# Kernel tuning notes

Hardware: AMD Instinct MI355X
Metric: run time of the kernel (lower is better)

## Reference

```python
import jax, jax.numpy as jnp
import numpy as np

N_SPK = 2048
M_UTT = 16
D_EMB = 512
EPS = 1e-8  # torch cosine_similarity eps


def setup_inputs() -> dict:
    key = jax.random.key(0)
    k1, = jax.random.split(key, 1)
    speaker_vectors = jax.random.normal(k1, (N_SPK * M_UTT, D_EMB), dtype=jnp.float32)
    return {
        "speaker_vectors": speaker_vectors,
        "w": jnp.float32(10.0),
        "b": jnp.float32(-5.0),
        "speakers": N_SPK,
    }


def _normalize(x):
    # torch.cosine_similarity clamps each norm at eps
    n = jnp.maximum(jnp.linalg.norm(x, axis=-1, keepdims=True), EPS)
    return x / n


def reference(speaker_vectors, w, b, speakers):
    N = speakers
    NM, D = speaker_vectors.shape
    M = NM // N
    v3 = speaker_vectors.reshape(N, M, D)
    ssum = v3.sum(axis=1)                         # [N, D] per-speaker sums
    C = ssum / M                                  # full centroids [N, D]
    C_min = (ssum[:, None, :] - v3) / (M - 1)     # leave-one-out centroids [N, M, D]

    vn = _normalize(speaker_vectors)              # [NM, D]
    # diagonal similarities: cos(C_min[j], v[j]) per utterance j
    S_diag = jnp.sum(_normalize(C_min.reshape(NM, D)) * vn, axis=-1)  # [NM]
    # full similarity matrix via one normalized matmul: [N, NM]
    S_full = _normalize(C) @ vn.T
    # replace each speaker's own block row entries with leave-one-out sims
    col_spk = jnp.arange(NM) // M                 # speaker id of each column
    same = col_spk[None, :] == jnp.arange(N)[:, None]  # [N, NM]
    S = jnp.where(same, S_diag[None, :], S_full)

    # L_j = -(w*S_diag_j + b) + log sum_n exp(w*S[n,j] + b)
    L = -(w * S_diag + b) + jax.nn.logsumexp(w * S + b, axis=0)
    return L.sum()
```

## Files before the change

### kernel.cpp

```cpp
#include <hip/hip_runtime.h>
#include <stdint.h>

#define N_SPK 2048
#define M_UTT 16
#define D_EMB 512
#define NM (N_SPK * M_UTT)
#define FP8_SCALE 16.0f

typedef __attribute__((ext_vector_type(4))) float f32x4;
typedef __attribute__((ext_vector_type(4))) int   i32x4;
typedef __attribute__((ext_vector_type(8))) int   i32x8;

__device__ __forceinline__ void async_copy16(const void* g, void* l) {
    __builtin_amdgcn_global_load_lds(
        (const __attribute__((address_space(1))) unsigned int*)g,
        (__attribute__((address_space(3))) unsigned int*)l,
        16, 0, 0);
}

__device__ __forceinline__ i32x8 ld_frag(const unsigned char* base, int s0) {
    i32x4 lo = *(const i32x4*)(base + s0 * 16);
    i32x4 hi = *(const i32x4*)(base + (s0 ^ 1) * 16);
    return __builtin_shufflevector(lo, hi, 0, 1, 2, 3, 4, 5, 6, 7);
}

__global__ __launch_bounds__(256) void prep_kernel(
    const float* __restrict__ V, const float* __restrict__ wp,
    const float* __restrict__ bp, unsigned char* __restrict__ Cn8,
    unsigned char* __restrict__ vn8, float* __restrict__ dterm,
    float* __restrict__ colsum, float* __restrict__ out)
{
    const int spk = blockIdx.x, t = threadIdx.x;
    const int wave = t >> 6, lane = t & 63;
    const float2* vb = (const float2*)(V + (size_t)spk * (M_UTT * D_EMB));

    __shared__ __align__(16) float red[32][264];
    __shared__ float red2[32];
    __shared__ float invs[M_UTT];
    __shared__ float wred[4];

    if (spk < 128) colsum[spk * 256 + t] = 0.f;
    if (spk == 0 && t == 0) out[0] = 0.f;

    float2 p[M_UTT];
#pragma unroll
    for (int m = 0; m < M_UTT; ++m) p[m] = vb[m * 256 + t];

    float2 ss = make_float2(0.f, 0.f);
#pragma unroll
    for (int m = 0; m < M_UTT; ++m) { ss.x += p[m].x; ss.y += p[m].y; }

    float cnp = ss.x * ss.x + ss.y * ss.y;
#pragma unroll
    for (int off = 32; off > 0; off >>= 1) cnp += __shfl_xor(cnp, off);
    if (lane == 0) wred[wave] = cnp;

#pragma unroll
    for (int m = 0; m < M_UTT; ++m) {
        red[m][t]         = ss.x * p[m].x + ss.y * p[m].y;
        red[m + M_UTT][t] = p[m].x * p[m].x + p[m].y * p[m].y;
    }
    __syncthreads();
    const float cn2 = wred[0] + wred[1] + wred[2] + wred[3];

    {
        const int r = t >> 3, s = t & 7;
        const float4* rp = (const float4*)red;
        float4 a = make_float4(0.f, 0.f, 0.f, 0.f);
#pragma unroll
        for (int k = 0; k < 8; ++k) {
            float4 q = rp[r * 66 + s + 8 * k];
            a.x += q.x; a.y += q.y; a.z += q.z; a.w += q.w;
        }
        float v1 = (a.x + a.y) + (a.z + a.w);
        v1 += __shfl_xor(v1, 1);
        v1 += __shfl_xor(v1, 2);
        v1 += __shfl_xor(v1, 4);
        if (s == 0) red2[r] = v1;
    }
    __syncthreads();

    if (t < M_UTT) {
        const float sv = red2[t], vv = red2[t + M_UTT];
        const float cc = cn2 - 2.f * sv + vv;
        const float cv = sv - vv;
        const float dc = fmaxf(sqrtf(fmaxf(cc, 0.f)) * (1.f / (M_UTT - 1)), 1e-8f) * (M_UTT - 1);
        const float dv = fmaxf(sqrtf(vv), 1e-8f);
        dterm[spk * M_UTT + t] = (*wp) * (cv / (dc * dv)) + (*bp);
        invs[t] = FP8_SCALE / dv;
    }
    __syncthreads();

    const float cs = FP8_SCALE / (M_UTT * fmaxf(sqrtf(cn2) * (1.f / M_UTT), 1e-8f));
    {
        int pk = __builtin_amdgcn_cvt_pk_fp8_f32(ss.x * cs, ss.y * cs, 0, false);
        ((unsigned short*)(Cn8 + (size_t)spk * D_EMB))[t] = (unsigned short)pk;
    }
#pragma unroll
    for (int m = 0; m < M_UTT; ++m) {
        const float iv = invs[m];
        int pk = __builtin_amdgcn_cvt_pk_fp8_f32(p[m].x * iv, p[m].y * iv, 0, false);
        ((unsigned short*)(vn8 + ((size_t)(spk * M_UTT + m)) * D_EMB))[t] = (unsigned short)pk;
    }
}

__global__ __launch_bounds__(256) void gemm_kernel(
    const unsigned char* __restrict__ Cn8, const unsigned char* __restrict__ vn8,
    const float* __restrict__ wp, const float* __restrict__ bp,
    float* __restrict__ colsum)
{
    __shared__ __align__(16) unsigned char As[2][128 * 128];
    __shared__ __align__(16) unsigned char Bs[2][128 * 128];
    __shared__ float csum[128];

    const int tid = threadIdx.x;
    const int w = tid >> 6, l = tid & 63;
    const int by = blockIdx.x;
    const int bx = blockIdx.y;
    const float wgt = (*wp) * (1.f / (FP8_SCALE * FP8_SCALE));
    const float bsc = *bp;

    if (tid < 128) csum[tid] = 0.f;

    const int srow = w * 32 + (l >> 3);
    const int sg   = (l & 7) ^ ((l >> 3) & 7);
    const unsigned char* Ab = Cn8 + (size_t)(by * 128 + srow) * D_EMB + sg * 16;
    const unsigned char* Bb = vn8 + (size_t)(bx * 128 + srow) * D_EMB + sg * 16;
    const int woff = (w * 32) * 128;

    const int wm = w & 1, wn = w >> 1;
    const int l16 = l & 15, q = l >> 4;
    const int s0 = (2 * q) ^ (l & 7);
    const int rdoff = (wm * 64 + l16) * 128;
    const int rdoffB = (wn * 64 + l16) * 128;

    f32x4 acc[4][4];
    const f32x4 z = {0.f, 0.f, 0.f, 0.f};
#pragma unroll
    for (int i = 0; i < 4; ++i)
#pragma unroll
        for (int j = 0; j < 4; ++j) acc[i][j] = z;

#pragma unroll
    for (int i = 0; i < 4; ++i) {
        async_copy16(Ab + (size_t)(i * 8) * D_EMB, &As[0][woff + i * 1024]);
        async_copy16(Bb + (size_t)(i * 8) * D_EMB, &Bs[0][woff + i * 1024]);
    }
    __syncthreads();

#pragma unroll
    for (int it = 0; it < 4; ++it) {
        const int cur = it & 1, nxt = cur ^ 1;
        if (it < 3) {
            const int kk = (it + 1) * 128;
#pragma unroll
            for (int i = 0; i < 4; ++i) {
                async_copy16(Ab + kk + (size_t)(i * 8) * D_EMB, &As[nxt][woff + i * 1024]);
                async_copy16(Bb + kk + (size_t)(i * 8) * D_EMB, &Bs[nxt][woff + i * 1024]);
            }
        }
        const unsigned char* Ard = &As[cur][rdoff];
        const unsigned char* Brd = &Bs[cur][rdoffB];
        i32x8 bfr[4];
#pragma unroll
        for (int j = 0; j < 4; ++j) bfr[j] = ld_frag(Brd + j * 2048, s0);
#pragma unroll
        for (int i = 0; i < 4; ++i) {
            i32x8 af = ld_frag(Ard + i * 2048, s0);
#pragma unroll
            for (int j = 0; j < 4; ++j)
                acc[i][j] = __builtin_amdgcn_mfma_scale_f32_16x16x128_f8f6f4(
                    af, bfr[j], acc[i][j], 0, 0, 0, 0x7F7F7F7F, 0, 0x7F7F7F7F);
        }
        __syncthreads();
    }

    const int rowg0 = by * 128 + wm * 64 + q * 4;
    const int colg0 = bx * 128 + wn * 64 + l16;
#pragma unroll
    for (int j = 0; j < 4; ++j) {
        const int colg = colg0 + j * 16;
        const int cspk = colg >> 4;
        float p = 0.f;
#pragma unroll
        for (int i = 0; i < 4; ++i) {
            const int rowg = rowg0 + i * 16;
#pragma unroll
            for (int r = 0; r < 4; ++r) {
                float e = __expf(wgt * acc[i][j][r] + bsc);
                p += (rowg + r == cspk) ? 0.f : e;
            }
        }
        p += __shfl_xor(p, 16);
        p += __shfl_xor(p, 32);
        if (q == 0) atomicAdd(&csum[wn * 64 + j * 16 + l16], p);
    }
    __syncthreads();
    if (tid < 128) atomicAdd(&colsum[bx * 128 + tid], csum[tid]);
}

__global__ __launch_bounds__(256) void finish_kernel(
    const float* __restrict__ dterm, const float* __restrict__ colsum,
    float* __restrict__ out)
{
    const int idx = blockIdx.x * 256 + threadIdx.x;
    const int stride = gridDim.x * 256;
    float local = 0.f;
    for (int j = idx; j < NM; j += stride) {
        float t = dterm[j];
        local += logf(colsum[j] + __expf(t)) - t;
    }
#pragma unroll
    for (int off = 32; off > 0; off >>= 1) local += __shfl_xor(local, off);
    __shared__ float wr[4];
    const int wave = threadIdx.x >> 6, lane = threadIdx.x & 63;
    if (lane == 0) wr[wave] = local;
    __syncthreads();
    if (threadIdx.x == 0) atomicAdd(out, wr[0] + wr[1] + wr[2] + wr[3]);
}

extern "C" void kernel_launch(void* const* d_in, const int* in_sizes, int n_in,
                              void* d_out, int out_size, void* d_ws, size_t ws_size,
                              hipStream_t stream) {
    const float* V  = (const float*)d_in[0];
    const float* wp = (const float*)d_in[1];
    const float* bp = (const float*)d_in[2];

    char* ws = (char*)d_ws;
    unsigned char* Cn8 = (unsigned char*)ws;
    unsigned char* vn8 = (unsigned char*)(ws + ((size_t)1 << 20));
    float* dterm  = (float*)(ws + ((size_t)17 << 20));
    float* colsum = dterm + NM;
    float* out    = (float*)d_out;

    prep_kernel<<<N_SPK, 256, 0, stream>>>(V, wp, bp, Cn8, vn8, dterm, colsum, out);
    gemm_kernel<<<dim3(N_SPK / 128, NM / 128), 256, 0, stream>>>(Cn8, vn8, wp, bp, colsum);
    finish_kernel<<<64, 256, 0, stream>>>(dterm, colsum, out);
}
```

Before: 154.8 us.

## Use one-wave prep blocks with shuffle reductions and single-buffer GEMM LDS

The prep kernel now runs one 64-thread wave per speaker. Each lane holds 8 floats per utterance, and all reductions use wave shuffles instead of LDS round trips and block barriers. The FP8 packing writes 4 bytes per conversion pair, so each store is 8 bytes. The GEMM drops LDS double buffering for a single buffer with barriers around each load, which halves shared memory and may raise occupancy, at the cost of losing the copy/compute overlap inside a block. The prep change also raises register pressure, since each lane holds 128 floats.

Result: no change. 157.8 us (+1.9%).

```diff
diff --git a/kernel.cpp b/kernel.cpp
--- a/kernel.cpp
+++ b/kernel.cpp
@@ -24,84 +24,81 @@
     return __builtin_shufflevector(lo, hi, 0, 1, 2, 3, 4, 5, 6, 7);
 }
 
-__global__ __launch_bounds__(256) void prep_kernel(
+__device__ __forceinline__ int pk_fp8x4(float a, float b, float c, float d) {
+    int v = __builtin_amdgcn_cvt_pk_fp8_f32(a, b, 0, false);
+    v = __builtin_amdgcn_cvt_pk_fp8_f32(c, d, v, true);
+    return v;
+}
+
+__device__ __forceinline__ float dot8(const float4& a0, const float4& a1,
+                                      const float4& b0, const float4& b1) {
+    return a0.x * b0.x + a0.y * b0.y + a0.z * b0.z + a0.w * b0.w +
+           a1.x * b1.x + a1.y * b1.y + a1.z * b1.z + a1.w * b1.w;
+}
+
+__global__ __launch_bounds__(64, 2) void prep_kernel(
     const float* __restrict__ V, const float* __restrict__ wp,
     const float* __restrict__ bp, unsigned char* __restrict__ Cn8,
     unsigned char* __restrict__ vn8, float* __restrict__ dterm,
     float* __restrict__ colsum, float* __restrict__ out)
 {
-    const int spk = blockIdx.x, t = threadIdx.x;
-    const int wave = t >> 6, lane = t & 63;
-    const float2* vb = (const float2*)(V + (size_t)spk * (M_UTT * D_EMB));
-
-    __shared__ __align__(16) float red[32][264];
-    __shared__ float red2[32];
-    __shared__ float invs[M_UTT];
-    __shared__ float wred[4];
-
-    if (spk < 128) colsum[spk * 256 + t] = 0.f;
-    if (spk == 0 && t == 0) out[0] = 0.f;
-
-    float2 p[M_UTT];
-#pragma unroll
-    for (int m = 0; m < M_UTT; ++m) p[m] = vb[m * 256 + t];
-
-    float2 ss = make_float2(0.f, 0.f);
-#pragma unroll
-    for (int m = 0; m < M_UTT; ++m) { ss.x += p[m].x; ss.y += p[m].y; }
-
-    float cnp = ss.x * ss.x + ss.y * ss.y;
-#pragma unroll
-    for (int off = 32; off > 0; off >>= 1) cnp += __shfl_xor(cnp, off);
-    if (lane == 0) wred[wave] = cnp;
-
+    const int spk = blockIdx.x, l = threadIdx.x;
+    const float4* vb = (const float4*)(V + (size_t)spk * (M_UTT * D_EMB));
+
+    if (spk < 512) colsum[spk * 64 + l] = 0.f;
+    if (spk == 0 && l == 0) out[0] = 0.f;
+
+    float4 r0[M_UTT], r1[M_UTT];
 #pragma unroll
     for (int m = 0; m < M_UTT; ++m) {
-        red[m][t]         = ss.x * p[m].x + ss.y * p[m].y;
-        red[m + M_UTT][t] = p[m].x * p[m].x + p[m].y * p[m].y;
-    }
-    __syncthreads();
-    const float cn2 = wred[0] + wred[1] + wred[2] + wred[3];
-
+        r0[m] = vb[m * 128 + 2 * l];
+        r1[m] = vb[m * 128 + 2 * l + 1];
+    }
+
+    float4 s0 = make_float4(0.f, 0.f, 0.f, 0.f), s1 = s0;
+#pragma unroll
+    for (int m = 0; m < M_UTT; ++m) {
+        s0.x += r0[m].x; s0.y += r0[m].y; s0.z += r0[m].z; s0.w += r0[m].w;
+        s1.x += r1[m].x; s1.y += r1[m].y; s1.z += r1[m].z; s1.w += r1[m].w;
+    }
+
+    float cn2 = dot8(s0, s1, s0, s1);
+#pragma unroll
+    for (int off = 32; off > 0; off >>= 1) cn2 += __shfl_xor(cn2, off);
+
+    const float wgt = *wp, bsc = *bp;
+
+    const float cs = FP8_SCALE / ((float)M_UTT * fmaxf(sqrtf(cn2) * (1.f / M_UTT), 1e-8f));
     {
-        const int r = t >> 3, s = t & 7;
-        const float4* rp = (const float4*)red;
-        float4 a = make_float4(0.f, 0.f, 0.f, 0.f);
-#pragma unroll
-        for (int k = 0; k < 8; ++k) {
-            float4 q = rp[r * 66 + s + 8 * k];
-            a.x += q.x; a.y += q.y; a.z += q.z; a.w += q.w;
-        }
-        float v1 = (a.x + a.y) + (a.z + a.w);
-        v1 += __shfl_xor(v1, 1);
-        v1 += __shfl_xor(v1, 2);
-        v1 += __shfl_xor(v1, 4);
-        if (s == 0) red2[r] = v1;
-    }
-    __syncthreads();
-
-    if (t < M_UTT) {
-        const float sv = red2[t], vv = red2[t + M_UTT];
+        int2 o;
+        o.x = pk_fp8x4(s0.x * cs, s0.y * cs, s0.z * cs, s0.w * cs);
+        o.y = pk_fp8x4(s1.x * cs, s1.y * cs, s1.z * cs, s1.w * cs);
+        ((int2*)(Cn8 + (size_t)spk * D_EMB))[l] = o;
+    }
+
+    float my_dt = 0.f;
+#pragma unroll
+    for (int m = 0; m < M_UTT; ++m) {
+        float sv = dot8(s0, s1, r0[m], r1[m]);
+        float vv = dot8(r0[m], r1[m], r0[m], r1[m]);
+#pragma unroll
+        for (int off = 32; off > 0; off >>= 1) {
+            sv += __shfl_xor(sv, off);
+            vv += __shfl_xor(vv, off);
+        }
         const float cc = cn2 - 2.f * sv + vv;
         const float cv = sv - vv;
         const float dc = fmaxf(sqrtf(fmaxf(cc, 0.f)) * (1.f / (M_UTT - 1)), 1e-8f) * (M_UTT - 1);
         const float dv = fmaxf(sqrtf(vv), 1e-8f);
-        dterm[spk * M_UTT + t] = (*wp) * (cv / (dc * dv)) + (*bp);
-        invs[t] = FP8_SCALE / dv;
-    }
-    __syncthreads();
-
-    const float cs = FP8_SCALE / (M_UTT * fmaxf(sqrtf(cn2) * (1.f / M_UTT), 1e-8f));
-    {
-        int pk = __builtin_amdgcn_cvt_pk_fp8_f32(ss.x * cs, ss.y * cs, 0, false);
-        ((unsigned short*)(Cn8 + (size_t)spk * D_EMB))[t] = (unsigned short)pk;
-    }
-#pragma unroll
-    for (int m = 0; m < M_UTT; ++m) {
-        const float iv = invs[m];
-        int pk = __builtin_amdgcn_cvt_pk_fp8_f32(p[m].x * iv, p[m].y * iv, 0, false);
-        ((unsigned short*)(vn8 + ((size_t)(spk * M_UTT + m)) * D_EMB))[t] = (unsigned short)pk;
-    }
+        const float dt = wgt * (cv / (dc * dv)) + bsc;
+        if (l == m) my_dt = dt;
+        const float iv = FP8_SCALE / dv;
+        int2 o;
+        o.x = pk_fp8x4(r0[m].x * iv, r0[m].y * iv, r0[m].z * iv, r0[m].w * iv);
+        o.y = pk_fp8x4(r1[m].x * iv, r1[m].y * iv, r1[m].z * iv, r1[m].w * iv);
+        ((int2*)(vn8 + ((size_t)(spk * M_UTT + m)) * D_EMB))[l] = o;
+    }
+    if (l < M_UTT) dterm[spk * M_UTT + l] = my_dt;
 }
 
 __global__ __launch_bounds__(256) void gemm_kernel(
@@ -109,8 +106,8 @@
     const float* __restrict__ wp, const float* __restrict__ bp,
     float* __restrict__ colsum)
 {
-    __shared__ __align__(16) unsigned char As[2][128 * 128];
-    __shared__ __align__(16) unsigned char Bs[2][128 * 128];
+    __shared__ __align__(16) unsigned char As[128 * 128];
+    __shared__ __align__(16) unsigned char Bs[128 * 128];
     __shared__ float csum[128];
 
     const int tid = threadIdx.x;
@@ -126,13 +123,14 @@
     const int sg   = (l & 7) ^ ((l >> 3) & 7);
     const unsigned char* Ab = Cn8 + (size_t)(by * 128 + srow) * D_EMB + sg * 16;
     const unsigned char* Bb = vn8 + (size_t)(bx * 128 + srow) * D_EMB + sg * 16;
-    const int woff = (w * 32) * 128;
+    unsigned char* AsW = As + (w * 32) * 128;
+    unsigned char* BsW = Bs + (w * 32) * 128;
 
     const int wm = w & 1, wn = w >> 1;
     const int l16 = l & 15, q = l >> 4;
     const int s0 = (2 * q) ^ (l & 7);
-    const int rdoff = (wm * 64 + l16) * 128;
-    const int rdoffB = (wn * 64 + l16) * 128;
+    const unsigned char* Ard = As + (wm * 64 + l16) * 128;
+    const unsigned char* Brd = Bs + (wn * 64 + l16) * 128;
 
     f32x4 acc[4][4];
     const f32x4 z = {0.f, 0.f, 0.f, 0.f};
@@ -141,26 +139,14 @@
 #pragma unroll
         for (int j = 0; j < 4; ++j) acc[i][j] = z;
 
-#pragma unroll
-    for (int i = 0; i < 4; ++i) {
-        async_copy16(Ab + (size_t)(i * 8) * D_EMB, &As[0][woff + i * 1024]);
-        async_copy16(Bb + (size_t)(i * 8) * D_EMB, &Bs[0][woff + i * 1024]);
-    }
-    __syncthreads();
-
-#pragma unroll
-    for (int it = 0; it < 4; ++it) {
-        const int cur = it & 1, nxt = cur ^ 1;
-        if (it < 3) {
-            const int kk = (it + 1) * 128;
-#pragma unroll
-            for (int i = 0; i < 4; ++i) {
-                async_copy16(Ab + kk + (size_t)(i * 8) * D_EMB, &As[nxt][woff + i * 1024]);
-                async_copy16(Bb + kk + (size_t)(i * 8) * D_EMB, &Bs[nxt][woff + i * 1024]);
-            }
-        }
-        const unsigned char* Ard = &As[cur][rdoff];
-        const unsigned char* Brd = &Bs[cur][rdoffB];
+    for (int kk = 0; kk < D_EMB; kk += 128) {
+        __syncthreads();
+#pragma unroll
+        for (int i = 0; i < 4; ++i) {
+            async_copy16(Ab + kk + (size_t)(i * 8) * D_EMB, AsW + i * 1024);
+            async_copy16(Bb + kk + (size_t)(i * 8) * D_EMB, BsW + i * 1024);
+        }
+        __syncthreads();
         i32x8 bfr[4];
 #pragma unroll
         for (int j = 0; j < 4; ++j) bfr[j] = ld_frag(Brd + j * 2048, s0);
@@ -172,7 +158,6 @@
                 acc[i][j] = __builtin_amdgcn_mfma_scale_f32_16x16x128_f8f6f4(
                     af, bfr[j], acc[i][j], 0, 0, 0, 0x7F7F7F7F, 0, 0x7F7F7F7F);
         }
-        __syncthreads();
     }
 
     const int rowg0 = by * 128 + wm * 64 + q * 4;
@@ -233,7 +218,7 @@
     float* colsum = dterm + NM;
     float* out    = (float*)d_out;
 
-    prep_kernel<<<N_SPK, 256, 0, stream>>>(V, wp, bp, Cn8, vn8, dterm, colsum, out);
+    prep_kernel<<<N_SPK, 64, 0, stream>>>(V, wp, bp, Cn8, vn8, dterm, colsum, out);
     gemm_kernel<<<dim3(N_SPK / 128, NM / 128), 256, 0, stream>>>(Cn8, vn8, wp, bp, colsum);
     finish_kernel<<<64, 256, 0, stream>>>(dterm, colsum, out);
 }
```
